# Performance work log

Hardware: AMD Instinct MI355X
Metric: run time of the kernel (lower is better)

Reference implementation:

```python
import jax, jax.numpy as jnp
import numpy as np

B, N, K = 4, 512, 10
PI_SCALE = 0.05  # keeps sum_k pi in (0, 0.5) so the [1e-8, 1] clamp does not saturate at 1
MCMC_KEY = jax.random.key(42)


def setup_inputs() -> dict:
    key = jax.random.key(0)
    k1, k2, k3, k4 = jax.random.split(key, 4)
    mu = jax.random.normal(k1, (B, N, K), dtype=jnp.float32)
    sig = jax.random.uniform(k2, (B, N, K), dtype=jnp.float32)
    pi = jax.random.uniform(k3, (B, N, K), dtype=jnp.float32) * PI_SCALE
    A_0 = jax.random.uniform(k4, (N, N), dtype=jnp.float32)
    return {"mu": mu, "sig": sig, "pi": pi, "A_0": A_0, "num_samples": 100}


def reference(mu, sig, pi, A_0, num_samples):
    b, n, k = mu.shape

    # Mixture-weighted proposal mean/std:  sum_k softmax(pi)_k * {mu,sig}_k
    component_probs = jax.nn.softmax(pi, axis=-1)          # [B,N,K]
    selected_mu = jnp.sum(component_probs * mu, axis=-1)    # [B,N]
    selected_sig = jnp.sum(component_probs * sig, axis=-1)  # [B,N]

    # edge_probs[b,i,j] = clamp(sum_k pi[b,i,k]) -- constant in j; hoisted out of the loop
    # since it depends only on pi (the torch code recomputes it every step).
    edge_probs = jnp.clip(jnp.sum(pi, axis=2), 1e-8, 1.0)[:, :, None]  # [B,N,1]
    log_ep = jnp.log(edge_probs)                                        # [B,N,1]
    log_1mep = jnp.log(1.0 - edge_probs)                                # [B,N,1]

    def log_likelihood(A):  # A: [B,N,N] -> [N]  (sum over dims 0,1 as in torch)
        return jnp.sum(A * log_ep + (1.0 - A) * log_1mep, axis=(0, 1))

    def step(carry, t):
        current_A, acc = carry
        kk = jax.random.fold_in(MCMC_KEY, t)
        k_noise, k_unif = jax.random.split(kk)
        noise = jax.random.normal(k_noise, (b, n), dtype=selected_mu.dtype)
        proposed_mu = selected_mu + noise * selected_sig              # [B,N]
        # sigmoid of rank-1 outer product: einsum('bnc,bmc->bnm') with c==1
        proposed_A = jax.nn.sigmoid(proposed_mu[:, :, None] * proposed_mu[:, None, :])
        ratio = jnp.mean(jnp.clip(jnp.exp(log_likelihood(proposed_A) - log_likelihood(current_A)), 0.0, 1.0))
        accept = jax.random.uniform(k_unif, (b,)) < ratio             # [B] bool
        current_A = jnp.where(accept[:, None, None], proposed_A, current_A)
        return (current_A, acc + current_A), None

    cur0 = jnp.broadcast_to(A_0, (b, n, n)).astype(mu.dtype)
    acc0 = jnp.zeros((b, n, n), dtype=mu.dtype)
    (_, acc), _ = jax.lax.scan(step, (cur0, acc0), jnp.arange(num_samples))
    return acc / num_samples
```

## Files before the change

kernel.cpp:

```cpp
#include <hip/hip_runtime.h>
#include <stdint.h>

#define T_STEPS 100
#define BB 4
#define NN 512
#define KK 10
#define TBTOT (T_STEPS * BB)
#define LLT_ELT ((size_t)TBTOT * NN)

__device__ __forceinline__ uint32_t rotl32(uint32_t v, int d) {
  return (v << d) | (v >> (32 - d));
}

__device__ __forceinline__ void tf2x32(uint32_t k0, uint32_t k1,
                                       uint32_t& x0, uint32_t& x1) {
  uint32_t k2 = k0 ^ k1 ^ 0x1BD11BDAu;
  x0 += k0; x1 += k1;
#define TFR(r) { x0 += x1; x1 = rotl32(x1, r); x1 ^= x0; }
  TFR(13) TFR(15) TFR(26) TFR(6)   x0 += k1; x1 += k2 + 1u;
  TFR(17) TFR(29) TFR(16) TFR(24)  x0 += k2; x1 += k0 + 2u;
  TFR(13) TFR(15) TFR(26) TFR(6)   x0 += k0; x1 += k1 + 3u;
  TFR(17) TFR(29) TFR(16) TFR(24)  x0 += k1; x1 += k2 + 4u;
  TFR(13) TFR(15) TFR(26) TFR(6)   x0 += k2; x1 += k0 + 5u;
#undef TFR
}

__device__ __forceinline__ float bits_to_u01(uint32_t bits) {
  return __fsub_rn(__uint_as_float((bits >> 9) | 0x3f800000u), 1.0f);
}

__device__ __forceinline__ float erfinv_f32(float x) {
  float w = -logf(__fmul_rn(__fsub_rn(1.0f, x), __fadd_rn(1.0f, x)));
  float p;
  if (w < 5.0f) {
    w = __fsub_rn(w, 2.5f);
    p = 2.81022636e-08f;
    p = __fadd_rn(__fmul_rn(p, w), 3.43273939e-07f);
    p = __fadd_rn(__fmul_rn(p, w), -3.5233877e-06f);
    p = __fadd_rn(__fmul_rn(p, w), -4.39150654e-06f);
    p = __fadd_rn(__fmul_rn(p, w), 0.00021858087f);
    p = __fadd_rn(__fmul_rn(p, w), -0.00125372503f);
    p = __fadd_rn(__fmul_rn(p, w), -0.00417768164f);
    p = __fadd_rn(__fmul_rn(p, w), 0.246640727f);
    p = __fadd_rn(__fmul_rn(p, w), 1.50140941f);
  } else {
    w = __fsub_rn(sqrtf(w), 3.0f);
    p = -0.000200214257f;
    p = __fadd_rn(__fmul_rn(p, w), 0.000100950558f);
    p = __fadd_rn(__fmul_rn(p, w), 0.00134934322f);
    p = __fadd_rn(__fmul_rn(p, w), -0.00367342844f);
    p = __fadd_rn(__fmul_rn(p, w), 0.00573950773f);
    p = __fadd_rn(__fmul_rn(p, w), -0.0076224613f);
    p = __fadd_rn(__fmul_rn(p, w), 0.00943887047f);
    p = __fadd_rn(__fmul_rn(p, w), 1.00167406f);
    p = __fadd_rn(__fmul_rn(p, w), 2.83297682f);
  }
  return __fmul_rn(p, x);
}

__device__ __forceinline__ float fast_sigmoid(float x) {
  float e = __expf(-x);
  return __builtin_amdgcn_rcpf(__fadd_rn(1.0f, e));
}

__global__ void prep_kernel(const float* __restrict__ mu,
                            const float* __restrict__ sig,
                            const float* __restrict__ pi,
                            float* __restrict__ sm, float* __restrict__ ss,
                            float* __restrict__ Lf) {
  int m = blockIdx.x * blockDim.x + threadIdx.x;
  if (m >= BB * NN) return;
  const float* pp = pi + m * KK;
  float mx = pp[0];
  for (int k = 1; k < KK; k++) mx = fmaxf(mx, pp[k]);
  float e[KK]; float s = 0.0f;
  for (int k = 0; k < KK; k++) { e[k] = expf(__fsub_rn(pp[k], mx)); s = __fadd_rn(s, e[k]); }
  float smv = 0.0f, ssv = 0.0f, eps = 0.0f;
  for (int k = 0; k < KK; k++) {
    float p = e[k] / s;
    smv = __fadd_rn(smv, __fmul_rn(p, mu[m * KK + k]));
    ssv = __fadd_rn(ssv, __fmul_rn(p, sig[m * KK + k]));
    eps = __fadd_rn(eps, pp[k]);
  }
  sm[m] = smv; ss[m] = ssv;
  float ep = fminf(fmaxf(eps, 1e-8f), 1.0f);
  float lep = logf(ep);
  float l1 = logf(__fsub_rn(1.0f, ep));
  Lf[m] = (float)((double)lep - (double)l1);
}

__global__ void rng_kernel(const float* __restrict__ sm,
                           const float* __restrict__ ss,
                           float* __restrict__ pm, float* __restrict__ uacc) {
  int id = blockIdx.x * blockDim.x + threadIdx.x;
  if (id >= T_STEPS * BB * NN) return;
  int t = id >> 11;
  int m = id & 2047;

  uint32_t kk0 = 0u, kk1 = (uint32_t)t;
  tf2x32(0u, 42u, kk0, kk1);
  uint32_t n0 = 0u, n1 = 0u; tf2x32(kk0, kk1, n0, n1);
  uint32_t y0 = 0u, y1 = (uint32_t)m;
  tf2x32(n0, n1, y0, y1);
  uint32_t bits = y0 ^ y1;

  float u01 = bits_to_u01(bits);
  const float lo = -0.99999994f;
  float u = fmaxf(lo, __fadd_rn(__fmul_rn(u01, 2.0f), lo));
  float z = __fmul_rn(1.41421356237309515f, erfinv_f32(u));
  pm[id] = __fadd_rn(sm[m], __fmul_rn(z, ss[m]));

  if (m < 4) {
    uint32_t u0 = 0u, u1 = 1u; tf2x32(kk0, kk1, u0, u1);
    uint32_t c0 = 0u, c1 = (uint32_t)m;
    tf2x32(u0, u1, c0, c1);
    uacc[t * 4 + m] = bits_to_u01(c0 ^ c1);
  }
}

template <int SPLIT>
__global__ __launch_bounds__(512) void ll_kernel(const float* __restrict__ pm,
                                                 const float* __restrict__ Lf,
                                                 const float* __restrict__ A0,
                                                 double* __restrict__ llt_p,
                                                 double* __restrict__ ll0_p) {
  constexpr int CH = NN / SPLIT;
  __shared__ float spm[CH];
  __shared__ float sLc[CH];
  int j = threadIdx.x;
  int bi = blockIdx.x;
  if (bi < TBTOT * SPLIT) {
    int tb = bi / SPLIT;
    int s = bi - tb * SPLIT;
    int b = tb & 3;
    int i0 = s * CH;
    if (j < CH) {
      spm[j] = pm[tb * NN + i0 + j];
      sLc[j] = Lf[b * NN + i0 + j];
    }
    float pmj = pm[tb * NN + j];
    __syncthreads();
    double acc = 0.0;
    #pragma unroll 8
    for (int i = 0; i < CH; i += 2) {
      float x0 = __fmul_rn(spm[i], pmj);
      float x1 = __fmul_rn(spm[i + 1], pmj);
      float t0 = __fmul_rn(fast_sigmoid(x0), sLc[i]);
      float t1 = __fmul_rn(fast_sigmoid(x1), sLc[i + 1]);
      acc += (double)__fadd_rn(t0, t1);
    }
    llt_p[(size_t)s * LLT_ELT + (size_t)tb * NN + j] = acc;
  } else {
    int bi2 = bi - TBTOT * SPLIT;
    int b = bi2 / SPLIT;
    int s = bi2 - b * SPLIT;
    int i0 = s * CH;
    if (j < CH) sLc[j] = Lf[b * NN + i0 + j];
    __syncthreads();
    double acc = 0.0;
    #pragma unroll 4
    for (int i = 0; i < CH; i++) {
      acc += (double)A0[(size_t)(i0 + i) * NN + j] * (double)sLc[i];
    }
    ll0_p[s * (BB * NN) + b * NN + j] = acc;
  }
}

template <int SPLIT>
__global__ __launch_bounds__(512) void combine_kernel(const double* __restrict__ llt_p,
                                                      const double* __restrict__ ll0_p,
                                                      double* __restrict__ llt,
                                                      double* __restrict__ ll0) {
  int bi = blockIdx.x;
  int j = threadIdx.x;
  if (bi < TBTOT) {
    size_t idx = (size_t)bi * NN + j;
    double a = llt_p[idx];
    #pragma unroll
    for (int s = 1; s < SPLIT; s++) a += llt_p[(size_t)s * LLT_ELT + idx];
    llt[idx] = a;
  } else {
    int idx = (bi - TBTOT) * NN + j;
    double a = ll0_p[idx];
    #pragma unroll
    for (int s = 1; s < SPLIT; s++) a += ll0_p[s * (BB * NN) + idx];
    ll0[idx] = a;
  }
}

#define CH_LOAD(BUF, T)                                                      \
  {                                                                          \
    _Pragma("unroll")                                                        \
    for (int b = 0; b < 4; b++)                                              \
      BUF[b] = llt2[((size_t)(T) * 4 + b) * 256 + g];                        \
  }

#define CH_STEP(BUF, T)                                                      \
  {                                                                          \
    float4 ua = sua[T];                                                      \
    double d0 = (BUF[0].x - cur[0].x) + (BUF[1].x - cur[1].x) +              \
                (BUF[2].x - cur[2].x) + (BUF[3].x - cur[3].x);               \
    double d1 = (BUF[0].y - cur[0].y) + (BUF[1].y - cur[1].y) +              \
                (BUF[2].y - cur[2].y) + (BUF[3].y - cur[3].y);               \
    float ps = __fadd_rn(fminf(__expf((float)d0), 1.0f),                     \
                         fminf(__expf((float)d1), 1.0f));                    \
    _Pragma("unroll")                                                        \
    for (int off = 32; off > 0; off >>= 1) ps += __shfl_xor(ps, off, 64);    \
    if ((g & 63) == 0) red[(T) & 1][g >> 6] = ps;                            \
    __syncthreads();                                                         \
    float ratio = (red[(T) & 1][0] + red[(T) & 1][1] + red[(T) & 1][2] +     \
                   red[(T) & 1][3]) * (1.0f / 512.0f);                       \
    if (ua.x < ratio) { st.x = (T); cur[0] = BUF[0]; }                       \
    if (ua.y < ratio) { st.y = (T); cur[1] = BUF[1]; }                       \
    if (ua.z < ratio) { st.z = (T); cur[2] = BUF[2]; }                       \
    if (ua.w < ratio) { st.w = (T); cur[3] = BUF[3]; }                       \
    if (g == 0) sst[T] = st;                                                 \
  }

__global__ __launch_bounds__(256, 1) void chain_kernel(const double* __restrict__ llt,
                                                       const double* __restrict__ ll0,
                                                       const float* __restrict__ uacc,
                                                       int* __restrict__ counts) {
  __shared__ float4 sua[T_STEPS];
  __shared__ int4 sst[T_STEPS];
  __shared__ int scnt[BB * (T_STEPS + 1)];
  __shared__ float red[2][4];
  int g = threadIdx.x;

  for (int t = g; t < T_STEPS; t += 256) {
    sua[t] = make_float4(uacc[4 * t], uacc[4 * t + 1],
                         uacc[4 * t + 2], uacc[4 * t + 3]);
  }

  const double2* llt2 = (const double2*)llt;
  const double2* ll02 = (const double2*)ll0;
  double2 cur[4];
  #pragma unroll
  for (int b = 0; b < 4; b++) cur[b] = ll02[b * 256 + g];
  int4 st = make_int4(-1, -1, -1, -1);

  double2 R0[4], R1[4], R2[4], R3[4];
  CH_LOAD(R0, 0)
  CH_LOAD(R1, 1)
  CH_LOAD(R2, 2)
  CH_LOAD(R3, 3)
  __syncthreads();

  for (int t = 0; t < T_STEPS; t += 4) {
    CH_STEP(R0, t)
    if (t + 4 < T_STEPS) CH_LOAD(R0, t + 4)
    CH_STEP(R1, t + 1)
    if (t + 5 < T_STEPS) CH_LOAD(R1, t + 5)
    CH_STEP(R2, t + 2)
    if (t + 6 < T_STEPS) CH_LOAD(R2, t + 6)
    CH_STEP(R3, t + 3)
    if (t + 7 < T_STEPS) CH_LOAD(R3, t + 7)
  }

  __syncthreads();
  for (int s = g; s < BB * (T_STEPS + 1); s += 256) scnt[s] = 0;
  __syncthreads();
  for (int t = g; t < T_STEPS; t += 256) {
    int4 s4 = sst[t];
    atomicAdd(&scnt[0 * (T_STEPS + 1) + s4.x + 1], 1);
    atomicAdd(&scnt[1 * (T_STEPS + 1) + s4.y + 1], 1);
    atomicAdd(&scnt[2 * (T_STEPS + 1) + s4.z + 1], 1);
    atomicAdd(&scnt[3 * (T_STEPS + 1) + s4.w + 1], 1);
  }
  __syncthreads();
  for (int s = g; s < BB * (T_STEPS + 1); s += 256) counts[s] = scnt[s];
}

__global__ __launch_bounds__(512) void out_kernel(const float* __restrict__ pm,
                                                  const float* __restrict__ A0,
                                                  const int* __restrict__ counts,
                                                  float* __restrict__ out) {
  __shared__ int scnt[T_STEPS + 1];
  int b = blockIdx.x >> 9;
  int i = blockIdx.x & 511;
  int j = threadIdx.x;
  if (j < T_STEPS + 1) scnt[j] = counts[b * (T_STEPS + 1) + j];
  __syncthreads();
  float r = (float)scnt[0] * A0[(size_t)i * NN + j];
  #pragma unroll 4
  for (int t = 0; t < T_STEPS; t++) {
    int c = scnt[t + 1];
    if (c) {
      float x = __fmul_rn(pm[(size_t)(t * BB + b) * NN + i],
                          pm[(size_t)(t * BB + b) * NN + j]);
      r += (float)c * fast_sigmoid(x);
    }
  }
  out[((size_t)b * NN + i) * NN + j] = r * 0.01f;
}

extern "C" void kernel_launch(void* const* d_in, const int* in_sizes, int n_in,
                              void* d_out, int out_size, void* d_ws, size_t ws_size,
                              hipStream_t stream) {
  const float* mu  = (const float*)d_in[0];
  const float* sig = (const float*)d_in[1];
  const float* pi  = (const float*)d_in[2];
  const float* A0  = (const float*)d_in[3];

  char* ws = (char*)d_ws;
  size_t off = 0;
  auto alloc = [&](size_t bytes) -> char* {
    char* p = ws + off;
    off += (bytes + 255) & ~(size_t)255;
    return p;
  };
  double* llt  = (double*)alloc(LLT_ELT * 8);
  double* ll0  = (double*)alloc(BB * NN * 8);
  float*  pm   = (float*)alloc(LLT_ELT * 4);
  float*  Lf   = (float*)alloc(BB * NN * 4);
  float*  sm   = (float*)alloc(BB * NN * 4);
  float*  ssv  = (float*)alloc(BB * NN * 4);
  float*  uacc = (float*)alloc(T_STEPS * 4 * 4);
  int*    cnts = (int*)alloc(BB * (T_STEPS + 1) * 4);
  size_t fixed_end = off;
  float*  outp = (float*)d_out;

  size_t part4 = 4 * LLT_ELT * 8 + 4 * BB * NN * 8 + 1024;
  size_t part2 = 2 * LLT_ELT * 8 + 2 * BB * NN * 8 + 1024;
  int split = (ws_size >= fixed_end + part4) ? 4
            : (ws_size >= fixed_end + part2) ? 2 : 1;

  double* llt_p;
  double* ll0_p;
  if (split > 1) {
    llt_p = (double*)alloc((size_t)split * LLT_ELT * 8);
    ll0_p = (double*)alloc((size_t)split * BB * NN * 8);
  } else {
    llt_p = llt;
    ll0_p = ll0;
  }

  prep_kernel<<<8, 256, 0, stream>>>(mu, sig, pi, sm, ssv, Lf);
  rng_kernel<<<(T_STEPS * BB * NN + 255) / 256, 256, 0, stream>>>(sm, ssv, pm, uacc);
  if (split == 4) {
    ll_kernel<4><<<(TBTOT + BB) * 4, 512, 0, stream>>>(pm, Lf, A0, llt_p, ll0_p);
    combine_kernel<4><<<TBTOT + BB, 512, 0, stream>>>(llt_p, ll0_p, llt, ll0);
  } else if (split == 2) {
    ll_kernel<2><<<(TBTOT + BB) * 2, 512, 0, stream>>>(pm, Lf, A0, llt_p, ll0_p);
    combine_kernel<2><<<TBTOT + BB, 512, 0, stream>>>(llt_p, ll0_p, llt, ll0);
  } else {
    ll_kernel<1><<<TBTOT + BB, 512, 0, stream>>>(pm, Lf, A0, llt_p, ll0_p);
  }
  chain_kernel<<<1, 256, 0, stream>>>(llt, ll0, uacc, cnts);
  out_kernel<<<BB * NN, 512, 0, stream>>>(pm, A0, cnts, outp);
}
```

Measured before the change: 150.8 us.

## Run MCMC chain in a single wavefront with precomputed per-step sums and DPP reduction

The chain kernel now runs as one 64-thread wavefront instead of four waves, so the per-step block reduction uses DPP adds and readlane, with no shared-memory round trip and no __syncthreads. The combine kernel also emits a per-step sum over batches (tsum). The chain keeps a running current total C, so each step computes its delta as tsum minus C instead of summing four batch differences. The goal is lower serial latency per MCMC step. The costs are more registers per thread for 4x4 double2 state, one less prefetch stage (three buffers instead of four), and an extra combine launch in the split==1 path.

Measured after the change: 154.1 us. +2.2%, slower.

```diff
diff --git a/kernel.cpp b/kernel.cpp
--- a/kernel.cpp
+++ b/kernel.cpp
@@ -63,6 +63,15 @@
   return __builtin_amdgcn_rcpf(__fadd_rn(1.0f, e));
 }
 
+template <int CTRL>
+__device__ __forceinline__ float dpp_add(float x) {
+  int v = __builtin_amdgcn_update_dpp(0, __float_as_int(x), CTRL, 0xF, 0xF, true);
+  return __fadd_rn(x, __int_as_float(v));
+}
+__device__ __forceinline__ float readlane_f(float x, int lane) {
+  return __int_as_float(__builtin_amdgcn_readlane(__float_as_int(x), lane));
+}
+
 __global__ void prep_kernel(const float* __restrict__ mu,
                             const float* __restrict__ sig,
                             const float* __restrict__ pi,
@@ -170,97 +179,140 @@
 __global__ __launch_bounds__(512) void combine_kernel(const double* __restrict__ llt_p,
                                                       const double* __restrict__ ll0_p,
                                                       double* __restrict__ llt,
-                                                      double* __restrict__ ll0) {
+                                                      double* __restrict__ ll0,
+                                                      double* __restrict__ tsum) {
   int bi = blockIdx.x;
   int j = threadIdx.x;
-  if (bi < TBTOT) {
-    size_t idx = (size_t)bi * NN + j;
-    double a = llt_p[idx];
+  if (bi < T_STEPS) {
+    double tj = 0.0;
     #pragma unroll
-    for (int s = 1; s < SPLIT; s++) a += llt_p[(size_t)s * LLT_ELT + idx];
-    llt[idx] = a;
+    for (int b = 0; b < BB; b++) {
+      size_t idx = ((size_t)bi * BB + b) * NN + j;
+      double a = llt_p[idx];
+      #pragma unroll
+      for (int s = 1; s < SPLIT; s++) a += llt_p[(size_t)s * LLT_ELT + idx];
+      llt[idx] = a;
+      tj += a;
+    }
+    tsum[(size_t)bi * NN + j] = tj;
   } else {
-    int idx = (bi - TBTOT) * NN + j;
-    double a = ll0_p[idx];
     #pragma unroll
-    for (int s = 1; s < SPLIT; s++) a += ll0_p[s * (BB * NN) + idx];
-    ll0[idx] = a;
-  }
-}
+    for (int b = 0; b < BB; b++) {
+      int idx = b * NN + j;
+      double a = ll0_p[idx];
+      #pragma unroll
+      for (int s = 1; s < SPLIT; s++) a += ll0_p[s * (BB * NN) + idx];
+      ll0[idx] = a;
+    }
+  }
+}
+
+struct ChainBuf {
+  double2 ll[4][4];
+  double2 ts[4];
+};
 
 #define CH_LOAD(BUF, T)                                                      \
   {                                                                          \
     _Pragma("unroll")                                                        \
-    for (int b = 0; b < 4; b++)                                              \
-      BUF[b] = llt2[((size_t)(T) * 4 + b) * 256 + g];                        \
+    for (int b = 0; b < 4; b++) {                                            \
+      _Pragma("unroll")                                                      \
+      for (int k = 0; k < 4; k++)                                            \
+        BUF.ll[b][k] = llt2[((size_t)(T) * 4 + b) * 256 + k * 64 + g];       \
+    }                                                                        \
+    _Pragma("unroll")                                                        \
+    for (int k = 0; k < 4; k++)                                              \
+      BUF.ts[k] = tsum2[(size_t)(T) * 256 + k * 64 + g];                     \
+  }
+
+#define CH_ACC(BUF, B)                                                       \
+  {                                                                          \
+    _Pragma("unroll")                                                        \
+    for (int k = 0; k < 4; k++) {                                            \
+      C[k].x += BUF.ll[B][k].x - cur[B][k].x;                                \
+      C[k].y += BUF.ll[B][k].y - cur[B][k].y;                                \
+      cur[B][k] = BUF.ll[B][k];                                              \
+    }                                                                        \
   }
 
 #define CH_STEP(BUF, T)                                                      \
   {                                                                          \
     float4 ua = sua[T];                                                      \
-    double d0 = (BUF[0].x - cur[0].x) + (BUF[1].x - cur[1].x) +              \
-                (BUF[2].x - cur[2].x) + (BUF[3].x - cur[3].x);               \
-    double d1 = (BUF[0].y - cur[0].y) + (BUF[1].y - cur[1].y) +              \
-                (BUF[2].y - cur[2].y) + (BUF[3].y - cur[3].y);               \
-    float ps = __fadd_rn(fminf(__expf((float)d0), 1.0f),                     \
-                         fminf(__expf((float)d1), 1.0f));                    \
-    _Pragma("unroll")                                                        \
-    for (int off = 32; off > 0; off >>= 1) ps += __shfl_xor(ps, off, 64);    \
-    if ((g & 63) == 0) red[(T) & 1][g >> 6] = ps;                            \
-    __syncthreads();                                                         \
-    float ratio = (red[(T) & 1][0] + red[(T) & 1][1] + red[(T) & 1][2] +     \
-                   red[(T) & 1][3]) * (1.0f / 512.0f);                       \
-    if (ua.x < ratio) { st.x = (T); cur[0] = BUF[0]; }                       \
-    if (ua.y < ratio) { st.y = (T); cur[1] = BUF[1]; }                       \
-    if (ua.z < ratio) { st.z = (T); cur[2] = BUF[2]; }                       \
-    if (ua.w < ratio) { st.w = (T); cur[3] = BUF[3]; }                       \
+    float e0x = fminf(__expf((float)(BUF.ts[0].x - C[0].x)), 1.0f);          \
+    float e0y = fminf(__expf((float)(BUF.ts[0].y - C[0].y)), 1.0f);          \
+    float e1x = fminf(__expf((float)(BUF.ts[1].x - C[1].x)), 1.0f);          \
+    float e1y = fminf(__expf((float)(BUF.ts[1].y - C[1].y)), 1.0f);          \
+    float e2x = fminf(__expf((float)(BUF.ts[2].x - C[2].x)), 1.0f);          \
+    float e2y = fminf(__expf((float)(BUF.ts[2].y - C[2].y)), 1.0f);          \
+    float e3x = fminf(__expf((float)(BUF.ts[3].x - C[3].x)), 1.0f);          \
+    float e3y = fminf(__expf((float)(BUF.ts[3].y - C[3].y)), 1.0f);          \
+    float ps = __fadd_rn(__fadd_rn(__fadd_rn(e0x, e0y), __fadd_rn(e1x, e1y)),\
+                         __fadd_rn(__fadd_rn(e2x, e2y), __fadd_rn(e3x, e3y)));\
+    ps = dpp_add<0xB1>(ps);                 \
+    ps = dpp_add<0x4E>(ps);                 \
+    ps = dpp_add<0x141>(ps);     \
+    ps = dpp_add<0x140>(ps);     \
+    float s0 = readlane_f(ps, 0), s1 = readlane_f(ps, 16);                   \
+    float s2 = readlane_f(ps, 32), s3 = readlane_f(ps, 48);                  \
+    float tot = __fadd_rn(__fadd_rn(s0, s1), __fadd_rn(s2, s3));             \
+    float ratio = __fmul_rn(tot, 1.0f / 512.0f);                             \
+    if (ua.x < ratio) { st.x = (T); CH_ACC(BUF, 0) }                         \
+    if (ua.y < ratio) { st.y = (T); CH_ACC(BUF, 1) }                         \
+    if (ua.z < ratio) { st.z = (T); CH_ACC(BUF, 2) }                         \
+    if (ua.w < ratio) { st.w = (T); CH_ACC(BUF, 3) }                         \
     if (g == 0) sst[T] = st;                                                 \
   }
 
-__global__ __launch_bounds__(256, 1) void chain_kernel(const double* __restrict__ llt,
-                                                       const double* __restrict__ ll0,
-                                                       const float* __restrict__ uacc,
-                                                       int* __restrict__ counts) {
+__global__ __launch_bounds__(64) void chain_kernel(const double* __restrict__ llt,
+                                                   const double* __restrict__ tsum,
+                                                   const double* __restrict__ ll0,
+                                                   const float* __restrict__ uacc,
+                                                   int* __restrict__ counts) {
   __shared__ float4 sua[T_STEPS];
   __shared__ int4 sst[T_STEPS];
   __shared__ int scnt[BB * (T_STEPS + 1)];
-  __shared__ float red[2][4];
   int g = threadIdx.x;
 
-  for (int t = g; t < T_STEPS; t += 256) {
-    sua[t] = make_float4(uacc[4 * t], uacc[4 * t + 1],
-                         uacc[4 * t + 2], uacc[4 * t + 3]);
-  }
-
-  const double2* llt2 = (const double2*)llt;
-  const double2* ll02 = (const double2*)ll0;
-  double2 cur[4];
+  const float4* uacc4 = (const float4*)uacc;
+  for (int t = g; t < T_STEPS; t += 64) sua[t] = uacc4[t];
+
+  const double2* llt2  = (const double2*)llt;
+  const double2* tsum2 = (const double2*)tsum;
+  const double2* ll02  = (const double2*)ll0;
+
+  double2 cur[4][4];
   #pragma unroll
-  for (int b = 0; b < 4; b++) cur[b] = ll02[b * 256 + g];
+  for (int b = 0; b < 4; b++)
+    #pragma unroll
+    for (int k = 0; k < 4; k++) cur[b][k] = ll02[b * 256 + k * 64 + g];
+  double2 C[4];
+  #pragma unroll
+  for (int k = 0; k < 4; k++) {
+    C[k].x = (cur[0][k].x + cur[1][k].x) + (cur[2][k].x + cur[3][k].x);
+    C[k].y = (cur[0][k].y + cur[1][k].y) + (cur[2][k].y + cur[3][k].y);
+  }
   int4 st = make_int4(-1, -1, -1, -1);
 
-  double2 R0[4], R1[4], R2[4], R3[4];
+  ChainBuf R0, R1, R2;
   CH_LOAD(R0, 0)
   CH_LOAD(R1, 1)
   CH_LOAD(R2, 2)
-  CH_LOAD(R3, 3)
   __syncthreads();
 
-  for (int t = 0; t < T_STEPS; t += 4) {
+  for (int t = 0; t < 99; t += 3) {
     CH_STEP(R0, t)
-    if (t + 4 < T_STEPS) CH_LOAD(R0, t + 4)
+    CH_LOAD(R0, t + 3)
     CH_STEP(R1, t + 1)
-    if (t + 5 < T_STEPS) CH_LOAD(R1, t + 5)
+    if (t + 4 < T_STEPS) CH_LOAD(R1, t + 4)
     CH_STEP(R2, t + 2)
-    if (t + 6 < T_STEPS) CH_LOAD(R2, t + 6)
-    CH_STEP(R3, t + 3)
-    if (t + 7 < T_STEPS) CH_LOAD(R3, t + 7)
-  }
+    if (t + 5 < T_STEPS) CH_LOAD(R2, t + 5)
+  }
+  CH_STEP(R0, 99)
 
   __syncthreads();
-  for (int s = g; s < BB * (T_STEPS + 1); s += 256) scnt[s] = 0;
+  for (int s = g; s < BB * (T_STEPS + 1); s += 64) scnt[s] = 0;
   __syncthreads();
-  for (int t = g; t < T_STEPS; t += 256) {
+  for (int t = g; t < T_STEPS; t += 64) {
     int4 s4 = sst[t];
     atomicAdd(&scnt[0 * (T_STEPS + 1) + s4.x + 1], 1);
     atomicAdd(&scnt[1 * (T_STEPS + 1) + s4.y + 1], 1);
@@ -268,7 +320,7 @@
     atomicAdd(&scnt[3 * (T_STEPS + 1) + s4.w + 1], 1);
   }
   __syncthreads();
-  for (int s = g; s < BB * (T_STEPS + 1); s += 256) counts[s] = scnt[s];
+  for (int s = g; s < BB * (T_STEPS + 1); s += 64) counts[s] = scnt[s];
 }
 
 __global__ __launch_bounds__(512) void out_kernel(const float* __restrict__ pm,
@@ -311,6 +363,7 @@
   };
   double* llt  = (double*)alloc(LLT_ELT * 8);
   double* ll0  = (double*)alloc(BB * NN * 8);
+  double* tsum = (double*)alloc((size_t)T_STEPS * NN * 8);
   float*  pm   = (float*)alloc(LLT_ELT * 4);
   float*  Lf   = (float*)alloc(BB * NN * 4);
   float*  sm   = (float*)alloc(BB * NN * 4);
@@ -339,13 +392,14 @@
   rng_kernel<<<(T_STEPS * BB * NN + 255) / 256, 256, 0, stream>>>(sm, ssv, pm, uacc);
   if (split == 4) {
     ll_kernel<4><<<(TBTOT + BB) * 4, 512, 0, stream>>>(pm, Lf, A0, llt_p, ll0_p);
-    combine_kernel<4><<<TBTOT + BB, 512, 0, stream>>>(llt_p, ll0_p, llt, ll0);
+    combine_kernel<4><<<T_STEPS + 1, 512, 0, stream>>>(llt_p, ll0_p, llt, ll0, tsum);
   } else if (split == 2) {
     ll_kernel<2><<<(TBTOT + BB) * 2, 512, 0, stream>>>(pm, Lf, A0, llt_p, ll0_p);
-    combine_kernel<2><<<TBTOT + BB, 512, 0, stream>>>(llt_p, ll0_p, llt, ll0);
+    combine_kernel<2><<<T_STEPS + 1, 512, 0, stream>>>(llt_p, ll0_p, llt, ll0, tsum);
   } else {
     ll_kernel<1><<<TBTOT + BB, 512, 0, stream>>>(pm, Lf, A0, llt_p, ll0_p);
-  }
-  chain_kernel<<<1, 256, 0, stream>>>(llt, ll0, uacc, cnts);
+    combine_kernel<1><<<T_STEPS + 1, 512, 0, stream>>>(llt_p, ll0_p, llt, ll0, tsum);
+  }
+  chain_kernel<<<1, 64, 0, stream>>>(llt, tsum, ll0, uacc, cnts);
   out_kernel<<<BB * NN, 512, 0, stream>>>(pm, A0, cnts, outp);
 }
```
